# Performance work log

Measured on AMD Instinct MI355X. Metric: run time of the kernel, lower is better.

The kernel has to match this reference:

```python
import jax, jax.numpy as jnp
import numpy as np

BETA = 1.0
EPS = 1e-12  # F.normalize eps

def _normalize(x):
    # F.normalize(x, dim=1): x shape (B, N, 1)
    n = jnp.sqrt(jnp.sum(x * x, axis=1, keepdims=True))
    return x / jnp.maximum(n, EPS)

def _step(M, x):
    return _normalize(jnp.matmul(M, x))

def _eigval(M, x):
    # x^T M x / ||x||^2, x: (B, N, 1)
    Mx = jnp.matmul(M, x)                          # (B, N, 1)
    num = jnp.sum(Mx * x, axis=(1, 2))             # (B,)
    den = jnp.sum(x * x, axis=(1, 2))              # (B,)
    return num / den

def setup_inputs() -> dict:
    key = jax.random.key(0)
    kA, kx = jax.random.split(key)
    A = jax.random.normal(kA, (64, 512, 28, 28), dtype=jnp.float32)
    x0 = jax.random.normal(kx, (64, 512, 1), dtype=jnp.float32)
    return {"A": A, "x0": x0}

def reference(A, x0):
    B, C, H, W = A.shape
    Wm = A.reshape(B, C, H * W)                    # (B, C, HW)
    AAT = jnp.einsum('bcd,bed->bce', Wm, Wm)       # (B, C, C)

    # --- dominant_eigenvalue(AAT): first call initializes last_x (no grad, 3 iters) ---
    xi = _normalize(x0)
    for _ in range(3):
        xi = _step(AAT, xi)
    xi = jax.lax.stop_gradient(xi)                 # last_x after no-grad init
    x1 = _step(AAT, xi)                            # 1 differentiable iter
    largest = _eigval(AAT, x1)                     # (B,)
    last_x = jax.lax.stop_gradient(x1)             # self.last_x = x.detach()

    # --- dominant_eigenvalue(AAT - largest*I): reuses last_x, 1 iter ---
    I = jnp.eye(C, dtype=A.dtype)[None]            # (1, C, C)
    A2 = AAT - largest[:, None, None] * I
    x2 = _step(A2, last_x)
    tmp = _eigval(A2, x2)

    smallest = tmp + largest
    penalty = BETA * (largest / smallest - 1.0) ** 2
    return jnp.sum(penalty) / B
```

## Files before the change

### kernel.cpp

```cpp
#include <hip/hip_runtime.h>
#include <math.h>


#define BB 64
#define CC 512
#define DD 784
#define NCH 49
#define QTOT 196
#define F4PR 196
#define BF4 100352
#define FEPS 1e-12f

__device__ __forceinline__ void gload16(const float4* gp, float4* lp) {
    __builtin_amdgcn_global_load_lds(
        (const __attribute__((address_space(1))) void*)gp,
        (__attribute__((address_space(3))) void*)lp, 16, 0, 0);
}

__device__ __forceinline__ float blk_reduce(float s, float* red) {
    for (int off = 32; off; off >>= 1) s += __shfl_down(s, off, 64);
    int w = threadIdx.x >> 6;
    if ((threadIdx.x & 63) == 0) red[w] = s;
    __syncthreads();
    float t = red[0] + red[1] + red[2] + red[3];
    __syncthreads();
    return t;
}

__global__ __launch_bounds__(256, 6)
void k_repack(const float* __restrict__ A, float* __restrict__ T) {
    __shared__ float4 lds4[8 * F4PR];
    const int tid = threadIdx.x, lane = tid & 63, w = tid >> 6;
    const int b = blockIdx.y, R0 = blockIdx.x * 8;
    const float4* src4 = (const float4*)A + ((size_t)b * CC + R0) * F4PR;
#pragma unroll
    for (int i = 0; i < 6; i++)
        gload16(src4 + i * 256 + w * 64 + lane, lds4 + i * 256 + w * 64);
    if (w == 0 && lane < 32) gload16(src4 + 1536 + lane, lds4 + 1536);
    __syncthreads();
    float4* dst4 = (float4*)T + (size_t)b * BF4;
#pragma unroll
    for (int j = 0; j < 7; j++) {
        int idx = j * 256 + tid;
        if (idx < 8 * F4PR) {
            int chq = idx >> 3, i = idx & 7;
            dst4[(size_t)chq * CC + R0 + i] = lds4[i * F4PR + chq];
        }
    }
}

__global__ void k_norm(const float* __restrict__ in, const int nparts,
                       float* __restrict__ out) {
    __shared__ float red[4];
    int b = blockIdx.x;
    const float* ip = in + (size_t)b * nparts * CC;
    float v0 = 0.f, v1 = 0.f;
    for (int p = 0; p < nparts; p++) {
        v0 += ip[p * CC + threadIdx.x];
        v1 += ip[p * CC + threadIdx.x + 256];
    }
    float ss = blk_reduce(v0 * v0 + v1 * v1, red);
    float rn = 1.0f / fmaxf(sqrtf(ss), FEPS);
    float* op = out + (size_t)b * CC;
    op[threadIdx.x] = v0 * rn;
    op[threadIdx.x + 256] = v1 * rn;
}

template <bool RP>
__global__ __launch_bounds__(256, 4)
void k_step(const float* __restrict__ M, const float* __restrict__ xhat,
            float* __restrict__ vout) {
    __shared__ float xs[CC];
    __shared__ float vws[4][CC];

    const int tid = threadIdx.x;
    const int b = blockIdx.y, s = blockIdx.x;
    const int lane = tid & 63, w = tid >> 6;
    const int chq = s * 4 + w;
    const float4* Mb = (const float4*)M + (size_t)b * BF4;

    float4 a[8];
    if (RP) {
        const float4* g = Mb + (size_t)chq * CC + lane;
#pragma unroll
        for (int k = 0; k < 8; k++) a[k] = g[64 * k];
    } else {
        const float4* g = Mb + (size_t)lane * F4PR + chq;
#pragma unroll
        for (int k = 0; k < 8; k++) a[k] = g[(size_t)64 * k * F4PR];
    }

    const float* xp = xhat + (size_t)b * CC;
    xs[tid] = xp[tid];
    xs[tid + 256] = xp[tid + 256];
    __syncthreads();
    float xk[8];
#pragma unroll
    for (int k = 0; k < 8; k++) xk[k] = xs[lane + 64 * k];

    float4 ua = make_float4(0.f, 0.f, 0.f, 0.f);
#pragma unroll
    for (int k = 0; k < 8; k++) {
        ua.x += a[k].x * xk[k]; ua.y += a[k].y * xk[k];
        ua.z += a[k].z * xk[k]; ua.w += a[k].w * xk[k];
    }
#pragma unroll
    for (int off = 1; off < 64; off <<= 1) {
        ua.x += __shfl_xor(ua.x, off, 64);
        ua.y += __shfl_xor(ua.y, off, 64);
        ua.z += __shfl_xor(ua.z, off, 64);
        ua.w += __shfl_xor(ua.w, off, 64);
    }

    float vk[8];
#pragma unroll
    for (int k = 0; k < 8; k++)
        vk[k] = a[k].x * ua.x + a[k].y * ua.y + a[k].z * ua.z + a[k].w * ua.w;

#pragma unroll
    for (int k = 0; k < 8; k++) vws[w][lane + 64 * k] = vk[k];
    __syncthreads();
    float* vp = vout + ((size_t)b * NCH + s) * CC;
    vp[tid]       = vws[0][tid] + vws[1][tid] + vws[2][tid] + vws[3][tid];
    vp[tid + 256] = vws[0][tid + 256] + vws[1][tid + 256] +
                    vws[2][tid + 256] + vws[3][tid + 256];
}

__global__ void k_mid(const float* __restrict__ x1, const float* __restrict__ P,
                      float* __restrict__ acc, float* __restrict__ yhat) {
    __shared__ float red[4];
    int b = blockIdx.x;
    const float* pp = P + (size_t)b * NCH * CC;
    float m0 = 0.f, m1 = 0.f;
    for (int p = 0; p < NCH; p++) {
        m0 += pp[p * CC + threadIdx.x];
        m1 += pp[p * CC + threadIdx.x + 256];
    }
    const float* xp = x1 + (size_t)b * CC;
    float x10 = xp[threadIdx.x], x11 = xp[threadIdx.x + 256];
    float num = blk_reduce(m0 * x10 + m1 * x11, red);
    float den = blk_reduce(x10 * x10 + x11 * x11, red);
    float largest = num / den;
    float y0 = m0 - largest * x10, y1 = m1 - largest * x11;
    float ssy = blk_reduce(y0 * y0 + y1 * y1, red);
    float rn = 1.0f / fmaxf(sqrtf(ssy), FEPS);
    float* yp = yhat + (size_t)b * CC;
    yp[threadIdx.x] = y0 * rn;
    yp[threadIdx.x + 256] = y1 * rn;
    if (threadIdx.x == 0) acc[b * 8 + 0] = largest;
}

__global__ void k_fin2(const float* __restrict__ P, const float* __restrict__ yhat,
                       float* __restrict__ acc) {
    __shared__ float red[4];
    int b = blockIdx.x;
    const float* pp = P + (size_t)b * NCH * CC;
    float w0 = 0.f, w1 = 0.f;
    for (int p = 0; p < NCH; p++) {
        w0 += pp[p * CC + threadIdx.x];
        w1 += pp[p * CC + threadIdx.x + 256];
    }
    const float* yp = yhat + (size_t)b * CC;
    float y0 = yp[threadIdx.x], y1 = yp[threadIdx.x + 256];
    float ssy = blk_reduce(y0 * y0 + y1 * y1, red);
    float rn = 1.0f / fmaxf(sqrtf(ssy), FEPS);
    float x20 = y0 * rn, x21 = y1 * rn;
    float dotwx = blk_reduce(w0 * x20 + w1 * x21, red);
    float den2 = blk_reduce(x20 * x20 + x21 * x21, red);
    if (threadIdx.x == 0) { acc[b * 8 + 1] = dotwx; acc[b * 8 + 2] = den2; }
}

__global__ void k_out(const float* __restrict__ acc, float* __restrict__ out) {
    int b = threadIdx.x;
    float largest = acc[b * 8 + 0];
    float dotwx   = acc[b * 8 + 1];
    float den2    = acc[b * 8 + 2];
    float tmp = (dotwx - largest * den2) / den2;
    float smallest = tmp + largest;
    float r = largest / smallest - 1.0f;
    float pen = r * r;
    for (int off = 32; off; off >>= 1) pen += __shfl_down(pen, off, 64);
    if (b == 0) out[0] = pen / (float)BB;
}

extern "C" void kernel_launch(void* const* d_in, const int* in_sizes, int n_in,
                              void* d_out, int out_size, void* d_ws, size_t ws_size,
                              hipStream_t stream) {
    const float* A  = (const float*)d_in[0];
    const float* x0 = (const float*)d_in[1];
    float* out = (float*)d_out;
    float* ws = (float*)d_ws;

    float* acc = ws;
    float* X   = ws + 512;
    float* Y   = X + BB * CC;
    float* P   = Y + BB * CC;
    float* T   = P + (size_t)BB * NCH * CC;
    const size_t need =
        ((size_t)512 + 2 * BB * CC + (size_t)BB * NCH * CC +
         (size_t)BB * CC * DD) * sizeof(float);

    dim3 gS(NCH, BB);
    if (ws_size >= need) {
        k_repack<<<dim3(CC / 8, BB), 256, 0, stream>>>(A, T);
        k_norm<<<BB, 256, 0, stream>>>(x0, 1, X);
        k_step<true><<<gS, 256, 0, stream>>>(T, X, P);
        k_norm<<<BB, 256, 0, stream>>>(P, NCH, X);
        k_step<true><<<gS, 256, 0, stream>>>(T, X, P);
        k_norm<<<BB, 256, 0, stream>>>(P, NCH, X);
        k_step<true><<<gS, 256, 0, stream>>>(T, X, P);
        k_norm<<<BB, 256, 0, stream>>>(P, NCH, X);
        k_step<true><<<gS, 256, 0, stream>>>(T, X, P);
        k_norm<<<BB, 256, 0, stream>>>(P, NCH, X);
        k_step<true><<<gS, 256, 0, stream>>>(T, X, P);
        k_mid<<<BB, 256, 0, stream>>>(X, P, acc, Y);
        k_step<true><<<gS, 256, 0, stream>>>(T, Y, P);
        k_fin2<<<BB, 256, 0, stream>>>(P, Y, acc);
    } else {
        k_norm<<<BB, 256, 0, stream>>>(x0, 1, X);
        k_step<false><<<gS, 256, 0, stream>>>(A, X, P);
        k_norm<<<BB, 256, 0, stream>>>(P, NCH, X);
        k_step<false><<<gS, 256, 0, stream>>>(A, X, P);
        k_norm<<<BB, 256, 0, stream>>>(P, NCH, X);
        k_step<false><<<gS, 256, 0, stream>>>(A, X, P);
        k_norm<<<BB, 256, 0, stream>>>(P, NCH, X);
        k_step<false><<<gS, 256, 0, stream>>>(A, X, P);
        k_norm<<<BB, 256, 0, stream>>>(P, NCH, X);
        k_step<false><<<gS, 256, 0, stream>>>(A, X, P);
        k_mid<<<BB, 256, 0, stream>>>(X, P, acc, Y);
        k_step<false><<<gS, 256, 0, stream>>>(A, Y, P);
        k_fin2<<<BB, 256, 0, stream>>>(P, Y, acc);
    }
    k_out<<<1, 64, 0, stream>>>(acc, out);
}
```

Measured before the change: 332.0 us.

## Retile repack into 64-channel blocks with swizzled LDS transpose

The repack kernel now transposes 64-row by 28-quad tiles through an XOR-swizzled LDS buffer, using register loads in place of direct global-to-LDS loads. This produces a blocked layout in which each k-slice of a channel block is contiguous, so both the repack writes and the step kernel's strided reads become fully coalesced 1KB runs. The step kernel is adjusted to the new layout, loads x with float4, reads x from LDS inside the FMA loop, and raises its occupancy hint. The main risk is whether the new block layout and the higher occupancy hint actually improve bandwidth for the dominant repack and step kernels.

```diff
diff --git a/kernel.cpp b/kernel.cpp
--- a/kernel.cpp
+++ b/kernel.cpp
@@ -6,16 +6,11 @@
 #define CC 512
 #define DD 784
 #define NCH 49
-#define QTOT 196
 #define F4PR 196
 #define BF4 100352
+#define QT 28
+#define CBS 12544
 #define FEPS 1e-12f
-
-__device__ __forceinline__ void gload16(const float4* gp, float4* lp) {
-    __builtin_amdgcn_global_load_lds(
-        (const __attribute__((address_space(1))) void*)gp,
-        (__attribute__((address_space(3))) void*)lp, 16, 0, 0);
-}
 
 __device__ __forceinline__ float blk_reduce(float s, float* red) {
     for (int off = 32; off; off >>= 1) s += __shfl_down(s, off, 64);
@@ -27,25 +22,31 @@
     return t;
 }
 
-__global__ __launch_bounds__(256, 6)
+__global__ __launch_bounds__(256, 5)
 void k_repack(const float* __restrict__ A, float* __restrict__ T) {
-    __shared__ float4 lds4[8 * F4PR];
-    const int tid = threadIdx.x, lane = tid & 63, w = tid >> 6;
-    const int b = blockIdx.y, R0 = blockIdx.x * 8;
-    const float4* src4 = (const float4*)A + ((size_t)b * CC + R0) * F4PR;
-#pragma unroll
-    for (int i = 0; i < 6; i++)
-        gload16(src4 + i * 256 + w * 64 + lane, lds4 + i * 256 + w * 64);
-    if (w == 0 && lane < 32) gload16(src4 + 1536 + lane, lds4 + 1536);
-    __syncthreads();
-    float4* dst4 = (float4*)T + (size_t)b * BF4;
+    __shared__ float4 lds4[64 * QT];
+    const int tid = threadIdx.x;
+    const int b = blockIdx.y, tile = blockIdx.x;
+    const int cb = tile / 7, qt = tile % 7;
+    const int R0 = cb * 64, q0 = qt * QT;
+    const int r = tid >> 2, qg = tid & 3;
+    const float4* src = (const float4*)A +
+        ((size_t)b * CC + R0 + r) * F4PR + q0 + qg * 7;
+    float4 a[7];
+#pragma unroll
+    for (int j = 0; j < 7; j++) a[j] = src[j];
+    const int xr = (r >> 2) & 3;
+#pragma unroll
+    for (int j = 0; j < 7; j++)
+        lds4[r * QT + ((qg * 7 + j) ^ xr)] = a[j];
+    __syncthreads();
+    float4* dst = (float4*)T + (size_t)b * BF4 + (size_t)cb * CBS +
+                  (size_t)q0 * 64;
 #pragma unroll
     for (int j = 0; j < 7; j++) {
         int idx = j * 256 + tid;
-        if (idx < 8 * F4PR) {
-            int chq = idx >> 3, i = idx & 7;
-            dst4[(size_t)chq * CC + R0 + i] = lds4[i * F4PR + chq];
-        }
+        int chq = idx >> 6, i = idx & 63;
+        dst[idx] = lds4[i * QT + (chq ^ ((i >> 2) & 3))];
     }
 }
 
@@ -67,7 +68,7 @@
 }
 
 template <bool RP>
-__global__ __launch_bounds__(256, 4)
+__global__ __launch_bounds__(256, 6)
 void k_step(const float* __restrict__ M, const float* __restrict__ xhat,
             float* __restrict__ vout) {
     __shared__ float xs[CC];
@@ -81,28 +82,25 @@
 
     float4 a[8];
     if (RP) {
-        const float4* g = Mb + (size_t)chq * CC + lane;
-#pragma unroll
-        for (int k = 0; k < 8; k++) a[k] = g[64 * k];
+        const float4* g = Mb + (size_t)chq * 64 + lane;
+#pragma unroll
+        for (int k = 0; k < 8; k++) a[k] = g[(size_t)k * CBS];
     } else {
         const float4* g = Mb + (size_t)lane * F4PR + chq;
 #pragma unroll
         for (int k = 0; k < 8; k++) a[k] = g[(size_t)64 * k * F4PR];
     }
 
-    const float* xp = xhat + (size_t)b * CC;
-    xs[tid] = xp[tid];
-    xs[tid + 256] = xp[tid + 256];
-    __syncthreads();
-    float xk[8];
-#pragma unroll
-    for (int k = 0; k < 8; k++) xk[k] = xs[lane + 64 * k];
+    const float4* xp4 = (const float4*)(xhat + (size_t)b * CC);
+    if (tid < 128) ((float4*)xs)[tid] = xp4[tid];
+    __syncthreads();
 
     float4 ua = make_float4(0.f, 0.f, 0.f, 0.f);
 #pragma unroll
     for (int k = 0; k < 8; k++) {
-        ua.x += a[k].x * xk[k]; ua.y += a[k].y * xk[k];
-        ua.z += a[k].z * xk[k]; ua.w += a[k].w * xk[k];
+        float x = xs[lane + 64 * k];
+        ua.x += a[k].x * x; ua.y += a[k].y * x;
+        ua.z += a[k].z * x; ua.w += a[k].w * x;
     }
 #pragma unroll
     for (int off = 1; off < 64; off <<= 1) {
@@ -202,7 +200,7 @@
 
     dim3 gS(NCH, BB);
     if (ws_size >= need) {
-        k_repack<<<dim3(CC / 8, BB), 256, 0, stream>>>(A, T);
+        k_repack<<<dim3(56, BB), 256, 0, stream>>>(A, T);
         k_norm<<<BB, 256, 0, stream>>>(x0, 1, X);
         k_step<true><<<gS, 256, 0, stream>>>(T, X, P);
         k_norm<<<BB, 256, 0, stream>>>(P, NCH, X);
```

Result: no change. 333.3 us (+0.4%).
